# Optimization experiments

Measured on AMD Instinct MI355X. Metric: run time of the kernel, lower is better.

The kernel has to match this reference:

```python
import jax, jax.numpy as jnp
import numpy as np

EPS = 1e-8
LN_EPS = 1e-5
NEG = -1e9
H, E, D, P = 4, 32, 8, 64          # heads, embed_dim, head_dim, particles (= input_dim)
N_LAYERS, N_CLS = 4, 2
N_BATCH = 2048
F_EXTRA = 60                        # x feature channels; F_EXTRA + 4 == P == input_dim


def _ln(x):
    m = jnp.mean(x, -1, keepdims=True)
    v = jnp.mean((x - m) ** 2, -1, keepdims=True)
    return (x - m) * jax.lax.rsqrt(v + LN_EPS)


def _lin(x, w, b):
    return x @ w.T + b


def _gelu(x):
    return jax.nn.gelu(x, approximate=False)


def _mha(q_in, kv, in_w, in_b, out_w, out_b, attn_bias, kpm):
    # torch nn.MultiheadAttention, batch_first=False. q_in: (L,N,E), kv: (S,N,E)
    L, N, _ = q_in.shape
    S = kv.shape[0]
    q = _lin(q_in, in_w[:E], in_b[:E]) * (D ** -0.5)
    k = _lin(kv, in_w[E:2 * E], in_b[E:2 * E])
    v = _lin(kv, in_w[2 * E:], in_b[2 * E:])
    q = q.reshape(L, N, H, D); k = k.reshape(S, N, H, D); v = v.reshape(S, N, H, D)
    s = jnp.einsum('lnhd,snhd->nhls', q, k)
    if attn_bias is not None:
        s = s + attn_bias.reshape(N, H, L, S)
    s = jnp.where(kpm[:, None, None, :], NEG, s)
    a = jax.nn.softmax(s, -1)
    o = jnp.einsum('nhls,snhd->lnhd', a, v).reshape(L, N, E)
    return _lin(o, out_w, out_b)


def _jet_features(v):
    # vectorized calculate_jet_features_; v: (N,4,P). All pair features are symmetric,
    # diagonal stays zero (python loop skipped i==j), features are detached.
    e, px, py, pz = v[:, 0], v[:, 1], v[:, 2], v[:, 3]
    pt = jnp.sqrt(px ** 2 + py ** 2 + EPS)
    y = 0.5 * jnp.log((e + pz + EPS) / (e - pz + EPS))
    phi = jnp.mod(jnp.arctan2(py, px + EPS), 2.0 * np.pi)   # already in [0, 2pi)
    r = lambda a: a[:, :, None]
    c = lambda a: a[:, None, :]
    dist = (r(px) + c(px)) ** 2 + (r(py) + c(py)) ** 2 + (r(pz) + c(pz)) ** 2
    delta = jnp.sqrt(jnp.abs((r(y) - c(y)) ** 2 + (r(phi) - c(phi)) ** 2))
    pmin = jnp.minimum(r(pt), c(pt))
    kt = pmin * delta
    z = pmin / (r(pt) + c(pt) + EPS)
    m2 = r(e) ** 2 + c(e) ** 2 - dist
    f = jnp.stack([delta, kt, z, m2], axis=1)               # (N,4,P,P)
    f = f * (1.0 - jnp.eye(v.shape[2], dtype=f.dtype))
    return jax.lax.stop_gradient(f)


def _conv2d(x, w, b, stride, pad):
    y = jax.lax.conv_general_dilated(x, w, (stride, stride), [(pad, pad), (pad, pad)],
                                     dimension_numbers=('NCHW', 'OIHW', 'NCHW'))
    return y + b[None, :, None, None]


def _forward(x, four_momenta, jet_inputs, bn_w, bn_b, e1_w, e1_b, e2_w, e2_b,
             c1_w, c1_b, c2_w, c2_b,
             pb_in_w, pb_in_b, pb_out_w, pb_out_b, pb_f1_w, pb_f1_b, pb_f2_w, pb_f2_b, pb_wres,
             cb_in_w, cb_in_b, cb_out_w, cb_out_b, cb_f1_w, cb_f1_b, cb_f2_w, cb_f2_b, cb_wres,
             cb_cattn, cls_token, norm_w, norm_b, m1_w, m1_b, mh_w, mh_b, mf_w, mf_b):
    N = x.shape[0]
    xc = jnp.concatenate([x, four_momenta], axis=1)                 # (N, P, P): channels == particles
    kpm = ~(jnp.arange(P)[None, :] < jet_inputs[:, 1][:, None])     # (N, P) True = padded key
    xb = jnp.transpose(xc, (0, 2, 1))                               # (N, C=P, L=input_dim)
    mu = jnp.mean(xb, axis=(0, 2), keepdims=True)
    var = jnp.var(xb, axis=(0, 2), keepdims=True)
    xb = (xb - mu) * jax.lax.rsqrt(var + LN_EPS) * bn_w[None, :, None] + bn_b[None, :, None]
    h = jnp.transpose(xb, (2, 0, 1))                                # (seq, N, P)
    h = _gelu(_lin(_ln(h), e1_w, e1_b))
    h = _gelu(_lin(_ln(h), e2_w, e2_b))                             # (P, N, E)
    # --- PairEmbed: pairwise kinematic features -> 2 convs -> per-head attention bias
    f = _jet_features(four_momenta)                                 # (N, 4, P, P)
    cpe = _conv2d(f, c1_w, c1_b, 4, 0)                              # (N, H, 16, 16)
    cpe = _conv2d(cpe, c2_w, c2_b, 2, 1)                            # (N, H, 9, 9)
    bias = cpe.reshape(N * H, 9, 9)
    bias = jnp.pad(bias, ((0, 0), (0, P - 9), (0, P - 9)))          # additive bias zero-padded to (N*H,P,P)
    # --- particle blocks
    for i in range(N_LAYERS):
        res = h
        a = _ln(h)
        a = _mha(a, a, pb_in_w[i], pb_in_b[i], pb_out_w[i], pb_out_b[i], bias, kpm)
        h = _ln(a) + res
        res = h
        g = _gelu(_lin(_ln(h), pb_f1_w[i], pb_f1_b[i]))
        g = _lin(_ln(g), pb_f2_w[i], pb_f2_b[i])
        h = g + pb_wres[i] * res
    # --- class-attention blocks
    kpm_cls = jnp.concatenate([jnp.zeros((N, 1), dtype=bool), kpm], axis=1)
    cls = jnp.broadcast_to(cls_token, (1, N, E))
    for i in range(N_CLS):
        res = cls
        u = _ln(jnp.concatenate([cls, h], axis=0))                  # pre_attn_norm on keys/values only
        a = _mha(cls, u, cb_in_w[i], cb_in_b[i], cb_out_w[i], cb_out_b[i], None, kpm_cls)
        # tbhd,h->tbdh then reshape flattens as (d, h) order, matching torch
        a = jnp.einsum('tbhd,h->tbdh', a.reshape(1, N, H, D), cb_cattn[i]).reshape(1, N, E)
        cls = _ln(a) + res
        res = cls
        g = _gelu(_lin(_ln(cls), cb_f1_w[i], cb_f1_b[i]))
        g = _lin(_ln(g), cb_f2_w[i], cb_f2_b[i])
        cls = g + cb_wres[i] * res
    # --- head: affine LayerNorm + MLP (the two transposes in MLP cancel)
    z = (_ln(cls) * norm_w + norm_b)[0]                             # (N, E)
    z = jax.nn.relu(_lin(z, m1_w, m1_b))
    z = jax.nn.relu(_lin(z, mh_w, mh_b))
    z = jax.nn.sigmoid(_lin(z, mf_w, mf_b))                         # (N, 1)
    return z.reshape(-1)


def setup_inputs():
    key = jax.random.key(0)
    ks = jax.random.split(key, 40)
    w = lambda k, s: (0.05 * jax.random.normal(k, s)).astype(jnp.float32)
    p3 = jax.random.normal(ks[0], (N_BATCH, 3, P), dtype=jnp.float32)
    en = jnp.sqrt(jnp.sum(p3 ** 2, axis=1, keepdims=True) + 0.1)    # physical: E > |pz|
    four_momenta = jnp.concatenate([en, p3], axis=1)
    return {
        'x': jax.random.normal(ks[1], (N_BATCH, F_EXTRA, P), dtype=jnp.float32),
        'four_momenta': four_momenta,
        'jet_inputs': jax.random.randint(ks[2], (N_BATCH, 2), 1, P + 1),
        'bn_w': jnp.ones((P,), jnp.float32), 'bn_b': jnp.zeros((P,), jnp.float32),
        'e1_w': w(ks[3], (64, P)), 'e1_b': w(ks[4], (64,)),
        'e2_w': w(ks[5], (E, 64)), 'e2_b': w(ks[6], (E,)),
        'c1_w': w(ks[7], (H, 4, 4, 4)), 'c1_b': w(ks[8], (H,)),
        'c2_w': w(ks[9], (H, H, 2, 2)), 'c2_b': w(ks[10], (H,)),
        'pb_in_w': w(ks[11], (N_LAYERS, 3 * E, E)), 'pb_in_b': w(ks[12], (N_LAYERS, 3 * E)),
        'pb_out_w': w(ks[13], (N_LAYERS, E, E)), 'pb_out_b': w(ks[14], (N_LAYERS, E)),
        'pb_f1_w': w(ks[15], (N_LAYERS, 2 * E, E)), 'pb_f1_b': w(ks[16], (N_LAYERS, 2 * E)),
        'pb_f2_w': w(ks[17], (N_LAYERS, E, 2 * E)), 'pb_f2_b': w(ks[18], (N_LAYERS, E)),
        'pb_wres': jnp.ones((N_LAYERS, E), jnp.float32),
        'cb_in_w': w(ks[19], (N_CLS, 3 * E, E)), 'cb_in_b': w(ks[20], (N_CLS, 3 * E)),
        'cb_out_w': w(ks[21], (N_CLS, E, E)), 'cb_out_b': w(ks[22], (N_CLS, E)),
        'cb_f1_w': w(ks[23], (N_CLS, 2 * E, E)), 'cb_f1_b': w(ks[24], (N_CLS, 2 * E)),
        'cb_f2_w': w(ks[25], (N_CLS, E, 2 * E)), 'cb_f2_b': w(ks[26], (N_CLS, E)),
        'cb_wres': jnp.ones((N_CLS, E), jnp.float32),
        'cb_cattn': jnp.ones((N_CLS, H), jnp.float32),
        'cls_token': w(ks[27], (1, 1, E)),
        'norm_w': jnp.ones((E,), jnp.float32), 'norm_b': jnp.zeros((E,), jnp.float32),
        'm1_w': w(ks[28], (32, E)), 'm1_b': w(ks[29], (32,)),
        'mh_w': w(ks[30], (32, 32)), 'mh_b': w(ks[31], (32,)),
        'mf_w': w(ks[32], (1, 32)), 'mf_b': w(ks[33], (1,)),
    }


def reference(x, four_momenta, jet_inputs, bn_w, bn_b, e1_w, e1_b, e2_w, e2_b,
              c1_w, c1_b, c2_w, c2_b,
              pb_in_w, pb_in_b, pb_out_w, pb_out_b, pb_f1_w, pb_f1_b, pb_f2_w, pb_f2_b, pb_wres,
              cb_in_w, cb_in_b, cb_out_w, cb_out_b, cb_f1_w, cb_f1_b, cb_f2_w, cb_f2_b, cb_wres,
              cb_cattn, cls_token, norm_w, norm_b, m1_w, m1_b, mh_w, mh_b, mf_w, mf_b):
    return _forward(x, four_momenta, jet_inputs, bn_w, bn_b, e1_w, e1_b, e2_w, e2_b,
                    c1_w, c1_b, c2_w, c2_b,
                    pb_in_w, pb_in_b, pb_out_w, pb_out_b, pb_f1_w, pb_f1_b, pb_f2_w, pb_f2_b, pb_wres,
                    cb_in_w, cb_in_b, cb_out_w, cb_out_b, cb_f1_w, cb_f1_b, cb_f2_w, cb_f2_b, cb_wres,
                    cb_cattn, cls_token, norm_w, norm_b, m1_w, m1_b, mh_w, mh_b, mf_w, mf_b)
```

## Files before the change

kernel.cpp:

```cpp
#include <hip/hip_runtime.h>


__device__ __forceinline__ float4 ld4(const float* p){ return *reinterpret_cast<const float4*>(p); }
__device__ __forceinline__ void st4(float* p, float4 v){ *reinterpret_cast<float4*>(p) = v; }
__device__ __forceinline__ float dot4(float4 a, float4 b){ return a.x*b.x + a.y*b.y + a.z*b.z + a.w*b.w; }
__device__ __forceinline__ float geluf(float v){ return 0.5f*v*(1.0f + erff(v*0.70710678118654752f)); }

__global__ void bn_stats_partial(const float* __restrict__ x, const float* __restrict__ fm,
                                 float* __restrict__ part) {
  int p  = threadIdx.x & 63;
  int rg = threadIdx.x >> 6;
  float s = 0.f, s2 = 0.f;
  for (int R = blockIdx.x*4 + rg; R < 2048*64; R += 1024) {
    int n_ = R >> 6, c = R & 63;
    float v = (c < 60) ? x[n_*3840 + c*64 + p] : fm[n_*256 + (c-60)*64 + p];
    s += v; s2 += v*v;
  }
  __shared__ float sm[256], sm2[256];
  sm[threadIdx.x] = s; sm2[threadIdx.x] = s2;
  __syncthreads();
  if (threadIdx.x < 64) {
    part[blockIdx.x*128 + p]      = sm[p]+sm[64+p]+sm[128+p]+sm[192+p];
    part[blockIdx.x*128 + 64 + p] = sm2[p]+sm2[64+p]+sm2[128+p]+sm2[192+p];
  }
}

__global__ void bn_stats_final(const float* __restrict__ part, float* __restrict__ stats) {
  int p = threadIdx.x;
  float s = 0.f, s2 = 0.f;
  for (int b = 0; b < 256; b++){ s += part[b*128+p]; s2 += part[b*128+64+p]; }
  float mean = s * (1.f/131072.f);
  float var  = s2 * (1.f/131072.f) - mean*mean;
  stats[p]      = mean;
  stats[64+p]   = rsqrtf(var + 1e-5f);
}

__device__ __forceinline__ void ln_rows32(const float* src, float* dst, int tid){
  int r = tid>>2, g = tid&3;
  const float* row = src + r*36 + g*8;
  float4 a = ld4(row), b = ld4(row+4);
  float s = a.x+a.y+a.z+a.w + b.x+b.y+b.z+b.w;
  s += __shfl_xor(s,1); s += __shfl_xor(s,2);
  float mean = s * 0.03125f;
  float4 da = make_float4(a.x-mean,a.y-mean,a.z-mean,a.w-mean);
  float4 db = make_float4(b.x-mean,b.y-mean,b.z-mean,b.w-mean);
  float q = dot4(da,da) + dot4(db,db);
  q += __shfl_xor(q,1); q += __shfl_xor(q,2);
  float irs = rsqrtf(q*0.03125f + 1e-5f);
  float* drow = dst + r*36 + g*8;
  st4(drow,   make_float4(da.x*irs, da.y*irs, da.z*irs, da.w*irs));
  st4(drow+4, make_float4(db.x*irs, db.y*irs, db.z*irs, db.w*irs));
}

__device__ __forceinline__ void ln_rows64(const float* src, float* dst, int tid){
  int r = tid>>2, g = tid&3;
  const float* row = src + r*68 + g*16;
  float4 v0 = ld4(row), v1 = ld4(row+4), v2 = ld4(row+8), v3 = ld4(row+12);
  float s = v0.x+v0.y+v0.z+v0.w + v1.x+v1.y+v1.z+v1.w
          + v2.x+v2.y+v2.z+v2.w + v3.x+v3.y+v3.z+v3.w;
  s += __shfl_xor(s,1); s += __shfl_xor(s,2);
  float mean = s * 0.015625f;
  float4 d0 = make_float4(v0.x-mean,v0.y-mean,v0.z-mean,v0.w-mean);
  float4 d1 = make_float4(v1.x-mean,v1.y-mean,v1.z-mean,v1.w-mean);
  float4 d2 = make_float4(v2.x-mean,v2.y-mean,v2.z-mean,v2.w-mean);
  float4 d3 = make_float4(v3.x-mean,v3.y-mean,v3.z-mean,v3.w-mean);
  float q = dot4(d0,d0)+dot4(d1,d1)+dot4(d2,d2)+dot4(d3,d3);
  q += __shfl_xor(q,1); q += __shfl_xor(q,2);
  float irs = rsqrtf(q*0.015625f + 1e-5f);
  float* drow = dst + r*68 + g*16;
  st4(drow,    make_float4(d0.x*irs,d0.y*irs,d0.z*irs,d0.w*irs));
  st4(drow+4,  make_float4(d1.x*irs,d1.y*irs,d1.z*irs,d1.w*irs));
  st4(drow+8,  make_float4(d2.x*irs,d2.y*irs,d2.z*irs,d2.w*irs));
  st4(drow+12, make_float4(d3.x*irs,d3.y*irs,d3.z*irs,d3.w*irs));
}

__global__ __launch_bounds__(256, 3) void k_embed(
    const float* __restrict__ x, const float* __restrict__ fm,
    const float* __restrict__ stats,
    const float* __restrict__ bn_w, const float* __restrict__ bn_b,
    const float* __restrict__ e1w, const float* __restrict__ e1b,
    const float* __restrict__ e2w, const float* __restrict__ e2b,
    const float* __restrict__ c1w_g, const float* __restrict__ c1b_g,
    const float* __restrict__ c2w_g, const float* __restrict__ c2b_g,
    float* __restrict__ G_h, float* __restrict__ G_bias)
{
  const int n   = blockIdx.x;
  const int tid = threadIdx.x;

  __shared__ __align__(16) float SX[64*68];
  __shared__ __align__(16) float SY[64*68];
  __shared__ __align__(16) float SW[4448];
  __shared__ float SSTAT[128];

  float* PQ  = SY;
  float* C1O = SY + 448;
  float* CW  = SY + 1472;

  if (tid < 64) {
    float mu = stats[tid], rs = stats[64+tid];
    float sc = rs * bn_w[tid];
    SSTAT[tid]      = sc;
    SSTAT[64+tid]   = bn_b[tid] - mu*sc;
  }
  if (tid < 64) {
    int p = tid;
    float e_  = fm[n*256 + p];
    float px_ = fm[n*256 + 64 + p];
    float py_ = fm[n*256 + 128 + p];
    float pz_ = fm[n*256 + 192 + p];
    float pt_ = sqrtf(px_*px_ + py_*py_ + 1e-8f);
    float y_  = 0.5f * logf((e_ + pz_ + 1e-8f) / (e_ - pz_ + 1e-8f));
    float ph_ = atan2f(py_, px_ + 1e-8f);
    if (ph_ < 0.f) ph_ += 6.283185307179586f;
    PQ[0*64+p]=e_; PQ[1*64+p]=px_; PQ[2*64+p]=py_; PQ[3*64+p]=pz_;
    PQ[4*64+p]=pt_; PQ[5*64+p]=y_; PQ[6*64+p]=ph_;
  }
  CW[tid] = c1w_g[tid];
  if (tid < 4)  CW[256+tid] = c1b_g[tid];
  if (tid < 64) CW[260+tid] = c2w_g[tid];
  if (tid < 4)  CW[324+tid] = c2b_g[tid];
  __syncthreads();

  {
    int ho = tid>>4, wo = tid&15;
    float a0=0.f,a1=0.f,a2=0.f,a3=0.f;
    #pragma unroll 1
    for (int kh=0; kh<4; kh++){
      int r = ho*4+kh;
      float er=PQ[r], pxr=PQ[64+r], pyr=PQ[128+r], pzr=PQ[192+r], ptr_=PQ[256+r], yr=PQ[320+r], phr=PQ[384+r];
      #pragma unroll
      for (int kw=0; kw<4; kw++){
        int c = wo*4+kw;
        if (r == c) continue;
        float ec=PQ[c], pxc=PQ[64+c], pyc=PQ[128+c], pzc=PQ[192+c], ptc=PQ[256+c], yc=PQ[320+c], phc=PQ[384+c];
        float dy = yr-yc, dp = phr-phc;
        float delta = sqrtf(fabsf(dy*dy + dp*dp));
        float pmin = fminf(ptr_, ptc);
        float kt = pmin * delta;
        float zz = pmin / (ptr_ + ptc + 1e-8f);
        float sx_ = pxr+pxc, sy_ = pyr+pyc, sz_ = pzr+pzc;
        float m2 = er*er + ec*ec - (sx_*sx_ + sy_*sy_ + sz_*sz_);
        int wb = kh*4+kw;
        a0 += delta*CW[0*64+wb] + kt*CW[0*64+16+wb] + zz*CW[0*64+32+wb] + m2*CW[0*64+48+wb];
        a1 += delta*CW[1*64+wb] + kt*CW[1*64+16+wb] + zz*CW[1*64+32+wb] + m2*CW[1*64+48+wb];
        a2 += delta*CW[2*64+wb] + kt*CW[2*64+16+wb] + zz*CW[2*64+32+wb] + m2*CW[2*64+48+wb];
        a3 += delta*CW[3*64+wb] + kt*CW[3*64+16+wb] + zz*CW[3*64+32+wb] + m2*CW[3*64+48+wb];
      }
    }
    C1O[0*256 + tid] = a0 + CW[256+0];
    C1O[1*256 + tid] = a1 + CW[256+1];
    C1O[2*256 + tid] = a2 + CW[256+2];
    C1O[3*256 + tid] = a3 + CW[256+3];
  }
  __syncthreads();

  for (int idx = tid; idx < 324; idx += 256) {
    int co = idx/81, rem = idx%81, i = rem/9, j = rem%9;
    float s = CW[324+co];
    #pragma unroll
    for (int ci=0; ci<4; ci++){
      #pragma unroll
      for (int kh=0; kh<2; kh++){
        int ri = 2*i - 1 + kh;
        if (ri < 0 || ri >= 16) continue;
        #pragma unroll
        for (int kw=0; kw<2; kw++){
          int cj = 2*j - 1 + kw;
          if (cj < 0 || cj >= 16) continue;
          s += CW[260 + co*16 + ci*4 + kh*2 + kw] * C1O[ci*256 + ri*16 + cj];
        }
      }
    }
    G_bias[n*324 + idx] = s;
  }
  {
    int p4 = (tid & 15) * 4;
    float sc0 = SSTAT[p4], sc1 = SSTAT[p4+1], sc2 = SSTAT[p4+2], sc3 = SSTAT[p4+3];
    float sh0 = SSTAT[64+p4], sh1 = SSTAT[64+p4+1], sh2 = SSTAT[64+p4+2], sh3 = SSTAT[64+p4+3];
    for (int c = tid>>4; c < 64; c += 16) {
      float4 v = (c < 60) ? ld4(x + n*3840 + c*64 + p4) : ld4(fm + n*256 + (c-60)*64 + p4);
      st4(&SX[c*68 + p4], make_float4(v.x*sc0+sh0, v.y*sc1+sh1, v.z*sc2+sh2, v.w*sc3+sh3));
    }
  }
  __syncthreads();

  ln_rows64(SX, SY, tid);
  for (int idx = tid; idx < 1024; idx += 256) st4(&SW[(idx>>4)*68 + (idx&15)*4], ld4(e1w + idx*4));
  if (tid < 64) SW[4352+tid] = e1b[tid];
  __syncthreads();

  {
    int tg = tid>>4, og = tid&15;
    float acc[4][4];
    #pragma unroll
    for (int o=0;o<4;o++){ float b = SW[4352+o*16+og];
      #pragma unroll
      for (int i=0;i<4;i++) acc[i][o] = b; }
    #pragma unroll 2
    for (int j=0;j<64;j+=4){
      float4 av[4], wv[4];
      #pragma unroll
      for (int i=0;i<4;i++) av[i] = ld4(SY + (tg*4+i)*68 + j);
      #pragma unroll
      for (int o=0;o<4;o++) wv[o] = ld4(SW + (o*16+og)*68 + j);
      #pragma unroll
      for (int i=0;i<4;i++)
        #pragma unroll
        for (int o=0;o<4;o++) acc[i][o] += dot4(av[i], wv[o]);
    }
    #pragma unroll
    for (int i=0;i<4;i++)
      #pragma unroll
      for (int o=0;o<4;o++) SX[(tg*4+i)*68 + o*16+og] = geluf(acc[i][o]);
  }
  __syncthreads();

  ln_rows64(SX, SY, tid);
  for (int idx = tid; idx < 512; idx += 256) st4(&SW[(idx>>4)*68 + (idx&15)*4], ld4(e2w + idx*4));
  if (tid < 32) SW[4352+tid] = e2b[tid];
  __syncthreads();

  {
    int tg = tid>>4, og = tid&15;
    float acc[4][2];
    #pragma unroll
    for (int o=0;o<2;o++){ float b = SW[4352+o*16+og];
      #pragma unroll
      for (int i=0;i<4;i++) acc[i][o] = b; }
    #pragma unroll 2
    for (int j=0;j<64;j+=4){
      float4 av[4], wv[2];
      #pragma unroll
      for (int i=0;i<4;i++) av[i] = ld4(SY + (tg*4+i)*68 + j);
      #pragma unroll
      for (int o=0;o<2;o++) wv[o] = ld4(SW + (o*16+og)*68 + j);
      #pragma unroll
      for (int i=0;i<4;i++)
        #pragma unroll
        for (int o=0;o<2;o++) acc[i][o] += dot4(av[i], wv[o]);
    }
    #pragma unroll
    for (int i=0;i<4;i++)
      #pragma unroll
      for (int o=0;o<2;o++) G_h[n*2048 + (tg*4+i)*32 + o*16+og] = geluf(acc[i][o]);
  }
}

__global__ __launch_bounds__(256, 3) void k_layer(
    const int* __restrict__ ji,
    const float* __restrict__ in_w,  const float* __restrict__ in_b,
    const float* __restrict__ out_w, const float* __restrict__ out_b,
    const float* __restrict__ f1w,   const float* __restrict__ f1b,
    const float* __restrict__ f2w,   const float* __restrict__ f2b,
    const float* __restrict__ wres,
    float* __restrict__ G_h, const float* __restrict__ G_bias)
{
  const int n   = blockIdx.x;
  const int tid = threadIdx.x;

  __shared__ __align__(16) float SH[64*36];
  __shared__ __align__(16) float SX[64*36];
  __shared__ __align__(16) float SY[64*68];
  __shared__ __align__(16) float SW[3584];
  __shared__ int s_njet;

  if (tid == 0) s_njet = ji[n*2+1];
  float b9[9];
  {
    int hh = tid>>6, l = tid&63;
    if (l < 9) {
      #pragma unroll
      for (int j=0;j<9;j++) b9[j] = G_bias[n*324 + hh*81 + l*9 + j];
    } else {
      #pragma unroll
      for (int j=0;j<9;j++) b9[j] = 0.f;
    }
  }
  for (int idx = tid; idx < 512; idx += 256) {
    float4 v = ld4(G_h + n*2048 + idx*4);
    int t = idx>>3, e = (idx&7)*4;
    st4(&SH[t*36 + e], v);
  }
  __syncthreads();

  ln_rows32(SH, SX, tid);
  for (int idx = tid; idx < 768; idx += 256) st4(&SW[(idx>>3)*36 + (idx&7)*4], ld4(in_w + idx*4));
  if (tid < 96) SW[3456+tid] = in_b[tid];
  __syncthreads();

  {
    int tg = tid>>4, og = tid&15;
    float acc[4][4];
    #pragma unroll
    for (int o=0;o<4;o++){ float b = SW[3456+32+o*16+og];
      #pragma unroll
      for (int i=0;i<4;i++) acc[i][o] = b; }
    #pragma unroll 2
    for (int j=0;j<32;j+=4){
      float4 av[4], wv[4];
      #pragma unroll
      for (int i=0;i<4;i++) av[i] = ld4(SX + (tg*4+i)*36 + j);
      #pragma unroll
      for (int o=0;o<4;o++) wv[o] = ld4(SW + (32+o*16+og)*36 + j);
      #pragma unroll
      for (int i=0;i<4;i++)
        #pragma unroll
        for (int o=0;o<4;o++) acc[i][o] += dot4(av[i], wv[o]);
    }
    #pragma unroll
    for (int i=0;i<4;i++)
      #pragma unroll
      for (int o=0;o<4;o++){
        int ew = 32 + o*16+og, t = tg*4+i;
        if (ew < 64) SY[(ew-32)*68 + t] = acc[i][o];
        else         SY[2176 + (ew-64)*68 + t] = acc[i][o];
      }
  }
  __syncthreads();

  float od[8];
  {
    int hh = tid>>6, l = tid&63;
    float qd[8];
    #pragma unroll
    for (int d=0;d<8;d++){
      int e = hh*8+d;
      float a_ = SW[3456+e];
      #pragma unroll
      for (int k=0;k<8;k++) a_ += dot4(ld4(SX + l*36 + k*4), ld4(SW + e*36 + k*4));
      qd[d] = a_ * 0.35355339059327373f;
    }
    int njet = s_njet;
    float m = -3.4e38f, lsum = 0.f;
    #pragma unroll
    for (int d=0;d<8;d++) od[d] = 0.f;
    #pragma unroll 1
    for (int s0 = 0; s0 < 64; s0 += 16) {
      float sc[16];
      #pragma unroll
      for (int j=0;j<16;j++) sc[j]=0.f;
      #pragma unroll
      for (int d=0;d<8;d++){
        const float* kr = SY + (hh*8+d)*68 + s0;
        float qv = qd[d];
        #pragma unroll
        for (int j=0;j<16;j+=4){
          float4 kv4 = ld4(kr+j);
          sc[j]  +=qv*kv4.x; sc[j+1]+=qv*kv4.y;
          sc[j+2]+=qv*kv4.z; sc[j+3]+=qv*kv4.w;
        }
      }
      float cm = -3.4e38f;
      #pragma unroll
      for (int j=0;j<16;j++){
        int s = s0+j;
        float a_ = sc[j];
        if (s0 == 0 && l < 9 && j < 9) a_ += b9[j];
        a_ = (s >= njet) ? -1000000000.0f : a_;
        sc[j] = a_;
        cm = fmaxf(cm, a_);
      }
      float nm = fmaxf(m, cm);
      float corr = __expf(m - nm);
      lsum *= corr;
      #pragma unroll
      for (int d=0;d<8;d++) od[d] *= corr;
      #pragma unroll
      for (int j=0;j<16;j++){ sc[j] = __expf(sc[j]-nm); lsum += sc[j]; }
      #pragma unroll
      for (int d=0;d<8;d++){
        const float* vr = SY + 2176 + (hh*8+d)*68 + s0;
        float a_ = 0.f;
        #pragma unroll
        for (int j=0;j<16;j+=4){
          float4 vv = ld4(vr+j);
          a_ += sc[j]*vv.x + sc[j+1]*vv.y + sc[j+2]*vv.z + sc[j+3]*vv.w;
        }
        od[d] += a_;
      }
      m = nm;
    }
    float inv = 1.f/lsum;
    #pragma unroll
    for (int d=0;d<8;d++) od[d] *= inv;
  }
  __syncthreads();
  {
    int hh = tid>>6, l = tid&63;
    st4(&SX[l*36 + hh*8],     make_float4(od[0],od[1],od[2],od[3]));
    st4(&SX[l*36 + hh*8 + 4], make_float4(od[4],od[5],od[6],od[7]));
  }
  for (int idx = tid; idx < 256; idx += 256) st4(&SW[(idx>>3)*36 + (idx&7)*4], ld4(out_w + idx*4));
  if (tid < 32) SW[3456+tid] = out_b[tid];
  __syncthreads();

  {
    int tg = tid>>4, og = tid&15;
    float acc[4][2];
    #pragma unroll
    for (int o=0;o<2;o++){ float b = SW[3456+o*16+og];
      #pragma unroll
      for (int i=0;i<4;i++) acc[i][o] = b; }
    #pragma unroll 2
    for (int j=0;j<32;j+=4){
      float4 av[4], wv[2];
      #pragma unroll
      for (int i=0;i<4;i++) av[i] = ld4(SX + (tg*4+i)*36 + j);
      #pragma unroll
      for (int o=0;o<2;o++) wv[o] = ld4(SW + (o*16+og)*36 + j);
      #pragma unroll
      for (int i=0;i<4;i++)
        #pragma unroll
        for (int o=0;o<2;o++) acc[i][o] += dot4(av[i], wv[o]);
    }
    #pragma unroll
    for (int i=0;i<4;i++)
      #pragma unroll
      for (int o=0;o<2;o++) SY[(tg*4+i)*36 + o*16+og] = acc[i][o];
  }
  __syncthreads();

  {
    int r = tid>>2, g = tid&3;
    const float* row = SY + r*36 + g*8;
    float4 a = ld4(row), b = ld4(row+4);
    float s = a.x+a.y+a.z+a.w + b.x+b.y+b.z+b.w;
    s += __shfl_xor(s,1); s += __shfl_xor(s,2);
    float mean = s * 0.03125f;
    float4 da = make_float4(a.x-mean,a.y-mean,a.z-mean,a.w-mean);
    float4 db = make_float4(b.x-mean,b.y-mean,b.z-mean,b.w-mean);
    float q = dot4(da,da) + dot4(db,db);
    q += __shfl_xor(q,1); q += __shfl_xor(q,2);
    float irs = rsqrtf(q*0.03125f + 1e-5f);
    float* hrow = SH + r*36 + g*8;
    float4 ha = ld4(hrow), hb = ld4(hrow+4);
    st4(hrow,   make_float4(da.x*irs+ha.x, da.y*irs+ha.y, da.z*irs+ha.z, da.w*irs+ha.w));
    st4(hrow+4, make_float4(db.x*irs+hb.x, db.y*irs+hb.y, db.z*irs+hb.z, db.w*irs+hb.w));
  }
  __syncthreads();

  ln_rows32(SH, SX, tid);
  for (int idx = tid; idx < 512; idx += 256) st4(&SW[(idx>>3)*36 + (idx&7)*4], ld4(f1w + idx*4));
  if (tid < 64) SW[3456+tid] = f1b[tid];
  __syncthreads();

  {
    int tg = tid>>4, og = tid&15;
    float acc[4][4];
    #pragma unroll
    for (int o=0;o<4;o++){ float b = SW[3456+o*16+og];
      #pragma unroll
      for (int i=0;i<4;i++) acc[i][o] = b; }
    #pragma unroll 2
    for (int j=0;j<32;j+=4){
      float4 av[4], wv[4];
      #pragma unroll
      for (int i=0;i<4;i++) av[i] = ld4(SX + (tg*4+i)*36 + j);
      #pragma unroll
      for (int o=0;o<4;o++) wv[o] = ld4(SW + (o*16+og)*36 + j);
      #pragma unroll
      for (int i=0;i<4;i++)
        #pragma unroll
        for (int o=0;o<4;o++) acc[i][o] += dot4(av[i], wv[o]);
    }
    #pragma unroll
    for (int i=0;i<4;i++)
      #pragma unroll
      for (int o=0;o<4;o++) SY[(tg*4+i)*68 + o*16+og] = geluf(acc[i][o]);
  }
  __syncthreads();

  {
    int r = tid>>2, g = tid&3;
    float* row = SY + r*68 + g*16;
    float4 v0 = ld4(row), v1 = ld4(row+4), v2 = ld4(row+8), v3 = ld4(row+12);
    float s = v0.x+v0.y+v0.z+v0.w + v1.x+v1.y+v1.z+v1.w
            + v2.x+v2.y+v2.z+v2.w + v3.x+v3.y+v3.z+v3.w;
    s += __shfl_xor(s,1); s += __shfl_xor(s,2);
    float mean = s * 0.015625f;
    float4 d0 = make_float4(v0.x-mean,v0.y-mean,v0.z-mean,v0.w-mean);
    float4 d1 = make_float4(v1.x-mean,v1.y-mean,v1.z-mean,v1.w-mean);
    float4 d2 = make_float4(v2.x-mean,v2.y-mean,v2.z-mean,v2.w-mean);
    float4 d3 = make_float4(v3.x-mean,v3.y-mean,v3.z-mean,v3.w-mean);
    float q = dot4(d0,d0)+dot4(d1,d1)+dot4(d2,d2)+dot4(d3,d3);
    q += __shfl_xor(q,1); q += __shfl_xor(q,2);
    float irs = rsqrtf(q*0.015625f + 1e-5f);
    st4(row,    make_float4(d0.x*irs,d0.y*irs,d0.z*irs,d0.w*irs));
    st4(row+4,  make_float4(d1.x*irs,d1.y*irs,d1.z*irs,d1.w*irs));
    st4(row+8,  make_float4(d2.x*irs,d2.y*irs,d2.z*irs,d2.w*irs));
    st4(row+12, make_float4(d3.x*irs,d3.y*irs,d3.z*irs,d3.w*irs));
  }
  for (int idx = tid; idx < 512; idx += 256) st4(&SW[(idx>>4)*68 + (idx&15)*4], ld4(f2w + idx*4));
  if (tid < 32){ SW[3456+tid] = f2b[tid]; SW[3488+tid] = wres[tid]; }
  __syncthreads();

  {
    int tg = tid>>4, og = tid&15;
    float acc[4][2];
    #pragma unroll
    for (int o=0;o<2;o++){ float b = SW[3456+o*16+og];
      #pragma unroll
      for (int i=0;i<4;i++) acc[i][o] = b; }
    #pragma unroll 2
    for (int j=0;j<64;j+=4){
      float4 av[4], wv[2];
      #pragma unroll
      for (int i=0;i<4;i++) av[i] = ld4(SY + (tg*4+i)*68 + j);
      #pragma unroll
      for (int o=0;o<2;o++) wv[o] = ld4(SW + (o*16+og)*68 + j);
      #pragma unroll
      for (int i=0;i<4;i++)
        #pragma unroll
        for (int o=0;o<2;o++) acc[i][o] += dot4(av[i], wv[o]);
    }
    #pragma unroll
    for (int i=0;i<4;i++)
      #pragma unroll
      for (int o=0;o<2;o++){
        int e = o*16+og, t = tg*4+i;
        G_h[n*2048 + t*32 + e] = acc[i][o] + SW[3488+e]*SH[t*36+e];
      }
  }
}

__global__ __launch_bounds__(256, 3) void k_cls(
    const int* __restrict__ ji,
    const float* __restrict__ cb_in_w, const float* __restrict__ cb_in_b,
    const float* __restrict__ cb_out_w, const float* __restrict__ cb_out_b,
    const float* __restrict__ cb_f1_w, const float* __restrict__ cb_f1_b,
    const float* __restrict__ cb_f2_w, const float* __restrict__ cb_f2_b,
    const float* __restrict__ cb_wres, const float* __restrict__ cb_cattn,
    const float* __restrict__ cls_tok, const float* __restrict__ norm_w, const float* __restrict__ norm_b,
    const float* __restrict__ m1w, const float* __restrict__ m1b,
    const float* __restrict__ mhw, const float* __restrict__ mhb,
    const float* __restrict__ mfw, const float* __restrict__ mfb,
    const float* __restrict__ G_h, float* __restrict__ out)
{
  const int n   = blockIdx.x;
  const int tid = threadIdx.x;

  __shared__ __align__(16) float SX[64*36];
  __shared__ __align__(16) float SY[64*68];
  __shared__ __align__(16) float SW[3584];
  __shared__ __align__(16) float SV[320];
  __shared__ __align__(16) float csh[32];
  __shared__ int s_njet;

  if (tid == 0) s_njet = ji[n*2+1];
  for (int idx = tid; idx < 512; idx += 256) {
    float4 v = ld4(G_h + n*2048 + idx*4);
    int t = idx>>3, e = (idx&7)*4;
    st4(&SX[t*36 + e], v);
  }
  __syncthreads();

  ln_rows32(SX, SX, tid);
  if (tid < 32) csh[tid] = cls_tok[tid];
  __syncthreads();

  #pragma unroll 1
  for (int cl = 0; cl < 2; cl++) {
    const float* iw = cb_in_w + cl*3072;
    const float* ib = cb_in_b + cl*96;

    if (tid < 32) {
      float v = csh[tid];
      float s = v;
      s += __shfl_xor(s,1); s += __shfl_xor(s,2); s += __shfl_xor(s,4); s += __shfl_xor(s,8); s += __shfl_xor(s,16);
      float mean = s * 0.03125f;
      float d = v - mean;
      float q = d*d;
      q += __shfl_xor(q,1); q += __shfl_xor(q,2); q += __shfl_xor(q,4); q += __shfl_xor(q,8); q += __shfl_xor(q,16);
      float irs = rsqrtf(q*0.03125f + 1e-5f);
      SV[tid] = d*irs;
    }
    for (int idx = tid; idx < 768; idx += 256) st4(&SW[(idx>>3)*36 + (idx&7)*4], ld4(iw + idx*4));
    if (tid < 96) SW[3456+tid] = ib[tid];
    __syncthreads();

    if (tid < 32) {
      int e = tid;
      float a_ = SW[3456+e];
      #pragma unroll
      for (int k=0;k<8;k++) a_ += dot4(ld4(&csh[k*4]), ld4(SW + e*36 + k*4));
      SV[32+e] = a_ * 0.35355339059327373f;
    }
    if (tid < 64) {
      int ew = 32 + tid;
      float a_ = SW[3456+ew];
      #pragma unroll
      for (int k=0;k<8;k++) a_ += dot4(ld4(SV + k*4), ld4(SW + ew*36 + k*4));
      if (ew < 64) SY[(ew-32)*68] = a_;
      else         SY[2176 + (ew-64)*68] = a_;
    }
    {
      int tg = tid>>4, og = tid&15;
      float acc[4][4];
      #pragma unroll
      for (int o=0;o<4;o++){ float b = SW[3456+32+o*16+og];
        #pragma unroll
        for (int i=0;i<4;i++) acc[i][o] = b; }
      #pragma unroll 2
      for (int j=0;j<32;j+=4){
        float4 av[4], wv[4];
        #pragma unroll
        for (int i=0;i<4;i++) av[i] = ld4(SX + (tg*4+i)*36 + j);
        #pragma unroll
        for (int o=0;o<4;o++) wv[o] = ld4(SW + (32+o*16+og)*36 + j);
        #pragma unroll
        for (int i=0;i<4;i++)
          #pragma unroll
          for (int o=0;o<4;o++) acc[i][o] += dot4(av[i], wv[o]);
      }
      #pragma unroll
      for (int i=0;i<4;i++)
        #pragma unroll
        for (int o=0;o<4;o++){
          int ew = 32 + o*16+og, s = tg*4+i + 1;
          if (ew < 64) SY[(ew-32)*68 + s] = acc[i][o];
          else         SY[2176 + (ew-64)*68 + s] = acc[i][o];
        }
    }
    __syncthreads();

    {
      int hh = tid>>6, l = tid&63;
      int njet = s_njet;
      float q8[8];
      #pragma unroll
      for (int d=0;d<8;d++) q8[d] = SV[32 + hh*8 + d];
      float sc_ = 0.f;
      #pragma unroll
      for (int d=0;d<8;d++) sc_ += q8[d]*SY[(hh*8+d)*68 + l];
      if (l > 0 && (l-1) >= njet) sc_ = -1000000000.0f;
      float sc64 = 0.f;
      if (l == 0){
        #pragma unroll
        for (int d=0;d<8;d++) sc64 += q8[d]*SY[(hh*8+d)*68 + 64];
        if (63 >= njet) sc64 = -1000000000.0f;
      }
      float mx = sc_;
      if (l == 0) mx = fmaxf(mx, sc64);
      mx = fmaxf(mx, __shfl_xor(mx,1));  mx = fmaxf(mx, __shfl_xor(mx,2));
      mx = fmaxf(mx, __shfl_xor(mx,4));  mx = fmaxf(mx, __shfl_xor(mx,8));
      mx = fmaxf(mx, __shfl_xor(mx,16)); mx = fmaxf(mx, __shfl_xor(mx,32));
      float p   = __expf(sc_ - mx);
      float p64 = (l==0) ? __expf(sc64 - mx) : 0.f;
      float ssum = p + p64;
      ssum += __shfl_xor(ssum,1); ssum += __shfl_xor(ssum,2); ssum += __shfl_xor(ssum,4);
      ssum += __shfl_xor(ssum,8); ssum += __shfl_xor(ssum,16); ssum += __shfl_xor(ssum,32);
      float inv = 1.f/ssum;
      #pragma unroll
      for (int d=0;d<8;d++){
        float term = p * SY[2176 + (hh*8+d)*68 + l];
        if (l == 0) term += p64 * SY[2176 + (hh*8+d)*68 + 64];
        term += __shfl_xor(term,1); term += __shfl_xor(term,2); term += __shfl_xor(term,4);
        term += __shfl_xor(term,8); term += __shfl_xor(term,16); term += __shfl_xor(term,32);
        if (l == 0) SV[64 + hh*8 + d] = term*inv;
      }
    }
    __syncthreads();

    if (tid < 32) {
      int e = tid;
      const float* wrow = cb_out_w + (cl*32 + e)*32;
      float a_ = cb_out_b[cl*32 + e];
      #pragma unroll
      for (int j=0;j<32;j++) a_ += SV[64+j]*wrow[j];
      float ca = cb_cattn[cl*4 + (e>>3)];
      SV[96 + (e&7)*4 + (e>>3)] = a_*ca;
    }
    if (tid < 32) {
      float v = SV[96+tid];
      float s = v;
      s += __shfl_xor(s,1); s += __shfl_xor(s,2); s += __shfl_xor(s,4); s += __shfl_xor(s,8); s += __shfl_xor(s,16);
      float mean = s * 0.03125f;
      float d = v - mean;
      float q = d*d;
      q += __shfl_xor(q,1); q += __shfl_xor(q,2); q += __shfl_xor(q,4); q += __shfl_xor(q,8); q += __shfl_xor(q,16);
      float irs = rsqrtf(q*0.03125f + 1e-5f);
      csh[tid] = d*irs + csh[tid];
    }
    if (tid < 32) {
      float v = csh[tid];
      float s = v;
      s += __shfl_xor(s,1); s += __shfl_xor(s,2); s += __shfl_xor(s,4); s += __shfl_xor(s,8); s += __shfl_xor(s,16);
      float mean = s * 0.03125f;
      float d = v - mean;
      float q = d*d;
      q += __shfl_xor(q,1); q += __shfl_xor(q,2); q += __shfl_xor(q,4); q += __shfl_xor(q,8); q += __shfl_xor(q,16);
      float irs = rsqrtf(q*0.03125f + 1e-5f);
      SV[tid] = d*irs;
    }
    if (tid < 64) {
      int o = tid;
      const float* wrow = cb_f1_w + (cl*64+o)*32;
      float a_ = cb_f1_b[cl*64+o];
      #pragma unroll
      for (int j=0;j<32;j++) a_ += SV[j]*wrow[j];
      SV[128+o] = geluf(a_);
    }
    if (tid < 64) {
      float v = SV[128+tid];
      float s = v;
      s += __shfl_xor(s,1); s += __shfl_xor(s,2); s += __shfl_xor(s,4); s += __shfl_xor(s,8);
      s += __shfl_xor(s,16); s += __shfl_xor(s,32);
      float mean = s * 0.015625f;
      float d = v - mean;
      float q = d*d;
      q += __shfl_xor(q,1); q += __shfl_xor(q,2); q += __shfl_xor(q,4); q += __shfl_xor(q,8);
      q += __shfl_xor(q,16); q += __shfl_xor(q,32);
      float irs = rsqrtf(q*0.015625f + 1e-5f);
      SV[192+tid] = d*irs;
    }
    if (tid < 32) {
      int e = tid;
      const float* wrow = cb_f2_w + (cl*32+e)*64;
      float a_ = cb_f2_b[cl*32+e];
      #pragma unroll
      for (int j=0;j<64;j++) a_ += SV[192+j]*wrow[j];
      csh[e] = a_ + cb_wres[cl*32+e]*csh[e];
    }
  }

  if (tid < 32) {
    float v = csh[tid];
    float s = v;
    s += __shfl_xor(s,1); s += __shfl_xor(s,2); s += __shfl_xor(s,4); s += __shfl_xor(s,8); s += __shfl_xor(s,16);
    float mean = s * 0.03125f;
    float d = v - mean;
    float q = d*d;
    q += __shfl_xor(q,1); q += __shfl_xor(q,2); q += __shfl_xor(q,4); q += __shfl_xor(q,8); q += __shfl_xor(q,16);
    float irs = rsqrtf(q*0.03125f + 1e-5f);
    SV[tid] = d*irs*norm_w[tid] + norm_b[tid];
  }
  if (tid < 32) {
    float a_ = m1b[tid];
    const float* wrow = m1w + tid*32;
    #pragma unroll
    for (int j=0;j<32;j++) a_ += SV[j]*wrow[j];
    SV[64+tid] = fmaxf(a_, 0.f);
  }
  if (tid < 32) {
    float a_ = mhb[tid];
    const float* wrow = mhw + tid*32;
    #pragma unroll
    for (int j=0;j<32;j++) a_ += SV[64+j]*wrow[j];
    SV[128+tid] = fmaxf(a_, 0.f);
  }
  if (tid == 0) {
    float a_ = mfb[0];
    #pragma unroll
    for (int j=0;j<32;j++) a_ += SV[128+j]*mfw[j];
    out[n] = 1.f/(1.f + expf(-a_));
  }
}

extern "C" void kernel_launch(void* const* d_in, const int* in_sizes, int n_in,
                              void* d_out, int out_size, void* d_ws, size_t ws_size,
                              hipStream_t stream) {
  (void)in_sizes; (void)n_in; (void)out_size; (void)ws_size;
  const float* x     = (const float*)d_in[0];
  const float* fm    = (const float*)d_in[1];
  const int*   ji    = (const int*)  d_in[2];
  const float* bn_w  = (const float*)d_in[3];
  const float* bn_b  = (const float*)d_in[4];
  const float* e1w   = (const float*)d_in[5];
  const float* e1b   = (const float*)d_in[6];
  const float* e2w   = (const float*)d_in[7];
  const float* e2b   = (const float*)d_in[8];
  const float* c1w   = (const float*)d_in[9];
  const float* c1b   = (const float*)d_in[10];
  const float* c2w   = (const float*)d_in[11];
  const float* c2b   = (const float*)d_in[12];
  const float* pb_in_w  = (const float*)d_in[13];
  const float* pb_in_b  = (const float*)d_in[14];
  const float* pb_out_w = (const float*)d_in[15];
  const float* pb_out_b = (const float*)d_in[16];
  const float* pb_f1_w  = (const float*)d_in[17];
  const float* pb_f1_b  = (const float*)d_in[18];
  const float* pb_f2_w  = (const float*)d_in[19];
  const float* pb_f2_b  = (const float*)d_in[20];
  const float* pb_wres  = (const float*)d_in[21];
  const float* cb_in_w  = (const float*)d_in[22];
  const float* cb_in_b  = (const float*)d_in[23];
  const float* cb_out_w = (const float*)d_in[24];
  const float* cb_out_b = (const float*)d_in[25];
  const float* cb_f1_w  = (const float*)d_in[26];
  const float* cb_f1_b  = (const float*)d_in[27];
  const float* cb_f2_w  = (const float*)d_in[28];
  const float* cb_f2_b  = (const float*)d_in[29];
  const float* cb_wres  = (const float*)d_in[30];
  const float* cb_cattn = (const float*)d_in[31];
  const float* cls_tok  = (const float*)d_in[32];
  const float* norm_w   = (const float*)d_in[33];
  const float* norm_b   = (const float*)d_in[34];
  const float* m1w      = (const float*)d_in[35];
  const float* m1b      = (const float*)d_in[36];
  const float* mhw      = (const float*)d_in[37];
  const float* mhb      = (const float*)d_in[38];
  const float* mfw      = (const float*)d_in[39];
  const float* mfb      = (const float*)d_in[40];

  float* part   = (float*)d_ws;
  float* stats  = part + 32768;
  float* G_h    = part + 40960;
  float* G_bias = G_h + 2048*2048;

  bn_stats_partial<<<256, 256, 0, stream>>>(x, fm, part);
  bn_stats_final<<<1, 64, 0, stream>>>(part, stats);
  k_embed<<<2048, 256, 0, stream>>>(x, fm, stats, bn_w, bn_b, e1w, e1b, e2w, e2b,
                                    c1w, c1b, c2w, c2b, G_h, G_bias);
  for (int li = 0; li < 4; li++) {
    k_layer<<<2048, 256, 0, stream>>>(ji,
        pb_in_w + li*3072, pb_in_b + li*96,
        pb_out_w + li*1024, pb_out_b + li*32,
        pb_f1_w + li*2048, pb_f1_b + li*64,
        pb_f2_w + li*2048, pb_f2_b + li*32,
        pb_wres + li*32, G_h, G_bias);
  }
  k_cls<<<2048, 256, 0, stream>>>(ji, cb_in_w, cb_in_b, cb_out_w, cb_out_b,
                                  cb_f1_w, cb_f1_b, cb_f2_w, cb_f2_b,
                                  cb_wres, cb_cattn, cls_tok, norm_w, norm_b,
                                  m1w, m1b, mhw, mhb, mfw, mfb, G_h, (float*)d_out);
}
```

Measured before the change: 537.5 us.

## Read weights directly from global memory instead of staging in LDS

Removes the shared-memory weight staging buffers in the embed, layer and cls kernels, so the GEMM-like loops load weights and biases straight from global memory through the cache. This also raises the launch-bounds occupancy hint from 3 to 4 blocks per CU, since the per-block LDS footprint shrinks. A barrier is added in the embed kernel because SX is now written in place, and another at the end of each cls-loop iteration. The trade-off is more global or L1 traffic and possible register pressure against fewer LDS copies and higher occupancy.

```diff
diff --git a/kernel.cpp b/kernel.cpp
--- a/kernel.cpp
+++ b/kernel.cpp
@@ -74,7 +74,7 @@
   st4(drow+12, make_float4(d3.x*irs,d3.y*irs,d3.z*irs,d3.w*irs));
 }
 
-__global__ __launch_bounds__(256, 3) void k_embed(
+__global__ __launch_bounds__(256, 4) void k_embed(
     const float* __restrict__ x, const float* __restrict__ fm,
     const float* __restrict__ stats,
     const float* __restrict__ bn_w, const float* __restrict__ bn_b,
@@ -89,7 +89,6 @@
 
   __shared__ __align__(16) float SX[64*68];
   __shared__ __align__(16) float SY[64*68];
-  __shared__ __align__(16) float SW[4448];
   __shared__ float SSTAT[128];
 
   float* PQ  = SY;
@@ -185,15 +184,13 @@
   __syncthreads();
 
   ln_rows64(SX, SY, tid);
-  for (int idx = tid; idx < 1024; idx += 256) st4(&SW[(idx>>4)*68 + (idx&15)*4], ld4(e1w + idx*4));
-  if (tid < 64) SW[4352+tid] = e1b[tid];
   __syncthreads();
 
   {
     int tg = tid>>4, og = tid&15;
     float acc[4][4];
     #pragma unroll
-    for (int o=0;o<4;o++){ float b = SW[4352+o*16+og];
+    for (int o=0;o<4;o++){ float b = e1b[o*16+og];
       #pragma unroll
       for (int i=0;i<4;i++) acc[i][o] = b; }
     #pragma unroll 2
@@ -202,12 +199,13 @@
       #pragma unroll
       for (int i=0;i<4;i++) av[i] = ld4(SY + (tg*4+i)*68 + j);
       #pragma unroll
-      for (int o=0;o<4;o++) wv[o] = ld4(SW + (o*16+og)*68 + j);
+      for (int o=0;o<4;o++) wv[o] = ld4(e1w + (o*16+og)*64 + j);
       #pragma unroll
       for (int i=0;i<4;i++)
         #pragma unroll
         for (int o=0;o<4;o++) acc[i][o] += dot4(av[i], wv[o]);
     }
+    __syncthreads();
     #pragma unroll
     for (int i=0;i<4;i++)
       #pragma unroll
@@ -216,15 +214,13 @@
   __syncthreads();
 
   ln_rows64(SX, SY, tid);
-  for (int idx = tid; idx < 512; idx += 256) st4(&SW[(idx>>4)*68 + (idx&15)*4], ld4(e2w + idx*4));
-  if (tid < 32) SW[4352+tid] = e2b[tid];
   __syncthreads();
 
   {
     int tg = tid>>4, og = tid&15;
     float acc[4][2];
     #pragma unroll
-    for (int o=0;o<2;o++){ float b = SW[4352+o*16+og];
+    for (int o=0;o<2;o++){ float b = e2b[o*16+og];
       #pragma unroll
       for (int i=0;i<4;i++) acc[i][o] = b; }
     #pragma unroll 2
@@ -233,7 +229,7 @@
       #pragma unroll
       for (int i=0;i<4;i++) av[i] = ld4(SY + (tg*4+i)*68 + j);
       #pragma unroll
-      for (int o=0;o<2;o++) wv[o] = ld4(SW + (o*16+og)*68 + j);
+      for (int o=0;o<2;o++) wv[o] = ld4(e2w + (o*16+og)*64 + j);
       #pragma unroll
       for (int i=0;i<4;i++)
         #pragma unroll
@@ -246,7 +242,7 @@
   }
 }
 
-__global__ __launch_bounds__(256, 3) void k_layer(
+__global__ __launch_bounds__(256, 4) void k_layer(
     const int* __restrict__ ji,
     const float* __restrict__ in_w,  const float* __restrict__ in_b,
     const float* __restrict__ out_w, const float* __restrict__ out_b,
@@ -261,7 +257,6 @@
   __shared__ __align__(16) float SH[64*36];
   __shared__ __align__(16) float SX[64*36];
   __shared__ __align__(16) float SY[64*68];
-  __shared__ __align__(16) float SW[3584];
   __shared__ int s_njet;
 
   if (tid == 0) s_njet = ji[n*2+1];
@@ -284,15 +279,13 @@
   __syncthreads();
 
   ln_rows32(SH, SX, tid);
-  for (int idx = tid; idx < 768; idx += 256) st4(&SW[(idx>>3)*36 + (idx&7)*4], ld4(in_w + idx*4));
-  if (tid < 96) SW[3456+tid] = in_b[tid];
   __syncthreads();
 
   {
     int tg = tid>>4, og = tid&15;
     float acc[4][4];
     #pragma unroll
-    for (int o=0;o<4;o++){ float b = SW[3456+32+o*16+og];
+    for (int o=0;o<4;o++){ float b = in_b[32+o*16+og];
       #pragma unroll
       for (int i=0;i<4;i++) acc[i][o] = b; }
     #pragma unroll 2
@@ -301,7 +294,7 @@
       #pragma unroll
       for (int i=0;i<4;i++) av[i] = ld4(SX + (tg*4+i)*36 + j);
       #pragma unroll
-      for (int o=0;o<4;o++) wv[o] = ld4(SW + (32+o*16+og)*36 + j);
+      for (int o=0;o<4;o++) wv[o] = ld4(in_w + (32+o*16+og)*32 + j);
       #pragma unroll
       for (int i=0;i<4;i++)
         #pragma unroll
@@ -325,9 +318,9 @@
     #pragma unroll
     for (int d=0;d<8;d++){
       int e = hh*8+d;
-      float a_ = SW[3456+e];
-      #pragma unroll
-      for (int k=0;k<8;k++) a_ += dot4(ld4(SX + l*36 + k*4), ld4(SW + e*36 + k*4));
+      float a_ = in_b[e];
+      #pragma unroll
+      for (int k=0;k<8;k++) a_ += dot4(ld4(SX + l*36 + k*4), ld4(in_w + e*32 + k*4));
       qd[d] = a_ * 0.35355339059327373f;
     }
     int njet = s_njet;
@@ -390,15 +383,13 @@
     st4(&SX[l*36 + hh*8],     make_float4(od[0],od[1],od[2],od[3]));
     st4(&SX[l*36 + hh*8 + 4], make_float4(od[4],od[5],od[6],od[7]));
   }
-  for (int idx = tid; idx < 256; idx += 256) st4(&SW[(idx>>3)*36 + (idx&7)*4], ld4(out_w + idx*4));
-  if (tid < 32) SW[3456+tid] = out_b[tid];
   __syncthreads();
 
   {
     int tg = tid>>4, og = tid&15;
     float acc[4][2];
     #pragma unroll
-    for (int o=0;o<2;o++){ float b = SW[3456+o*16+og];
+    for (int o=0;o<2;o++){ float b = out_b[o*16+og];
       #pragma unroll
       for (int i=0;i<4;i++) acc[i][o] = b; }
     #pragma unroll 2
@@ -407,7 +398,7 @@
       #pragma unroll
       for (int i=0;i<4;i++) av[i] = ld4(SX + (tg*4+i)*36 + j);
       #pragma unroll
-      for (int o=0;o<2;o++) wv[o] = ld4(SW + (o*16+og)*36 + j);
+      for (int o=0;o<2;o++) wv[o] = ld4(out_w + (o*16+og)*32 + j);
       #pragma unroll
       for (int i=0;i<4;i++)
         #pragma unroll
@@ -440,15 +431,13 @@
   __syncthreads();
 
   ln_rows32(SH, SX, tid);
-  for (int idx = tid; idx < 512; idx += 256) st4(&SW[(idx>>3)*36 + (idx&7)*4], ld4(f1w + idx*4));
-  if (tid < 64) SW[3456+tid] = f1b[tid];
   __syncthreads();
 
   {
     int tg = tid>>4, og = tid&15;
     float acc[4][4];
     #pragma unroll
-    for (int o=0;o<4;o++){ float b = SW[3456+o*16+og];
+    for (int o=0;o<4;o++){ float b = f1b[o*16+og];
       #pragma unroll
       for (int i=0;i<4;i++) acc[i][o] = b; }
     #pragma unroll 2
@@ -457,7 +446,7 @@
       #pragma unroll
       for (int i=0;i<4;i++) av[i] = ld4(SX + (tg*4+i)*36 + j);
       #pragma unroll
-      for (int o=0;o<4;o++) wv[o] = ld4(SW + (o*16+og)*36 + j);
+      for (int o=0;o<4;o++) wv[o] = ld4(f1w + (o*16+og)*32 + j);
       #pragma unroll
       for (int i=0;i<4;i++)
         #pragma unroll
@@ -490,15 +479,13 @@
     st4(row+8,  make_float4(d2.x*irs,d2.y*irs,d2.z*irs,d2.w*irs));
     st4(row+12, make_float4(d3.x*irs,d3.y*irs,d3.z*irs,d3.w*irs));
   }
-  for (int idx = tid; idx < 512; idx += 256) st4(&SW[(idx>>4)*68 + (idx&15)*4], ld4(f2w + idx*4));
-  if (tid < 32){ SW[3456+tid] = f2b[tid]; SW[3488+tid] = wres[tid]; }
   __syncthreads();
 
   {
     int tg = tid>>4, og = tid&15;
     float acc[4][2];
     #pragma unroll
-    for (int o=0;o<2;o++){ float b = SW[3456+o*16+og];
+    for (int o=0;o<2;o++){ float b = f2b[o*16+og];
       #pragma unroll
       for (int i=0;i<4;i++) acc[i][o] = b; }
     #pragma unroll 2
@@ -507,7 +494,7 @@
       #pragma unroll
       for (int i=0;i<4;i++) av[i] = ld4(SY + (tg*4+i)*68 + j);
       #pragma unroll
-      for (int o=0;o<2;o++) wv[o] = ld4(SW + (o*16+og)*68 + j);
+      for (int o=0;o<2;o++) wv[o] = ld4(f2w + (o*16+og)*64 + j);
       #pragma unroll
       for (int i=0;i<4;i++)
         #pragma unroll
@@ -518,12 +505,12 @@
       #pragma unroll
       for (int o=0;o<2;o++){
         int e = o*16+og, t = tg*4+i;
-        G_h[n*2048 + t*32 + e] = acc[i][o] + SW[3488+e]*SH[t*36+e];
+        G_h[n*2048 + t*32 + e] = acc[i][o] + wres[e]*SH[t*36+e];
       }
   }
 }
 
-__global__ __launch_bounds__(256, 3) void k_cls(
+__global__ __launch_bounds__(256, 4) void k_cls(
     const int* __restrict__ ji,
     const float* __restrict__ cb_in_w, const float* __restrict__ cb_in_b,
     const float* __restrict__ cb_out_w, const float* __restrict__ cb_out_b,
@@ -541,7 +528,6 @@
 
   __shared__ __align__(16) float SX[64*36];
   __shared__ __align__(16) float SY[64*68];
-  __shared__ __align__(16) float SW[3584];
   __shared__ __align__(16) float SV[320];
   __shared__ __align__(16) float csh[32];
   __shared__ int s_njet;
@@ -574,22 +560,20 @@
       float irs = rsqrtf(q*0.03125f + 1e-5f);
       SV[tid] = d*irs;
     }
-    for (int idx = tid; idx < 768; idx += 256) st4(&SW[(idx>>3)*36 + (idx&7)*4], ld4(iw + idx*4));
-    if (tid < 96) SW[3456+tid] = ib[tid];
     __syncthreads();
 
     if (tid < 32) {
       int e = tid;
-      float a_ = SW[3456+e];
-      #pragma unroll
-      for (int k=0;k<8;k++) a_ += dot4(ld4(&csh[k*4]), ld4(SW + e*36 + k*4));
+      float a_ = ib[e];
+      #pragma unroll
+      for (int k=0;k<8;k++) a_ += dot4(ld4(&csh[k*4]), ld4(iw + e*32 + k*4));
       SV[32+e] = a_ * 0.35355339059327373f;
     }
     if (tid < 64) {
       int ew = 32 + tid;
-      float a_ = SW[3456+ew];
-      #pragma unroll
-      for (int k=0;k<8;k++) a_ += dot4(ld4(SV + k*4), ld4(SW + ew*36 + k*4));
+      float a_ = ib[ew];
+      #pragma unroll
+      for (int k=0;k<8;k++) a_ += dot4(ld4(SV + k*4), ld4(iw + ew*32 + k*4));
       if (ew < 64) SY[(ew-32)*68] = a_;
       else         SY[2176 + (ew-64)*68] = a_;
     }
@@ -597,7 +581,7 @@
       int tg = tid>>4, og = tid&15;
       float acc[4][4];
       #pragma unroll
-      for (int o=0;o<4;o++){ float b = SW[3456+32+o*16+og];
+      for (int o=0;o<4;o++){ float b = ib[32+o*16+og];
         #pragma unroll
         for (int i=0;i<4;i++) acc[i][o] = b; }
       #pragma unroll 2
@@ -606,7 +590,7 @@
         #pragma unroll
         for (int i=0;i<4;i++) av[i] = ld4(SX + (tg*4+i)*36 + j);
         #pragma unroll
-        for (int o=0;o<4;o++) wv[o] = ld4(SW + (32+o*16+og)*36 + j);
+        for (int o=0;o<4;o++) wv[o] = ld4(iw + (32+o*16+og)*32 + j);
         #pragma unroll
         for (int i=0;i<4;i++)
           #pragma unroll
@@ -721,6 +705,7 @@
       for (int j=0;j<64;j++) a_ += SV[192+j]*wrow[j];
       csh[e] = a_ + cb_wres[cl*32+e]*csh[e];
     }
+    __syncthreads();
   }
 
   if (tid < 32) {
```

New measurement: 780.0 us. 45.1% more time.
